# Kernel optimization log

Measured on AMD Instinct MI355X. Metric: run time of the kernel, lower is better.

Reference implementation:

```python
import jax, jax.numpy as jnp
import numpy as np

B, C, S, W, H = 4, 512, 1, 64, 64
D = C // 8  # query/key channel dim from Conv2d(in_dim, in_dim // 8, 1)
N = W * H


def setup_inputs() -> dict:
    key = jax.random.key(0)
    ks = jax.random.split(key, 8)
    s_in = 1.0 / np.sqrt(C)
    return {
        "x": jax.random.normal(ks[0], (B, C, S, W, H), dtype=jnp.float32),
        "Wq": jax.random.normal(ks[1], (D, C), dtype=jnp.float32) * s_in,
        "bq": jax.random.normal(ks[2], (D,), dtype=jnp.float32) * 0.01,
        "Wk": jax.random.normal(ks[3], (D, C), dtype=jnp.float32) * s_in,
        "bk": jax.random.normal(ks[4], (D,), dtype=jnp.float32) * 0.01,
        "Wv": jax.random.normal(ks[5], (C, C), dtype=jnp.float32) * s_in,
        "bv": jax.random.normal(ks[6], (C,), dtype=jnp.float32) * 0.01,
        "gamma": jax.random.uniform(ks[7], (1,), dtype=jnp.float32),
        "crop_h": 64,
        "crop_w": 64,
    }


def reference(x, Wq, bq, Wk, bk, Wv, bv, gamma, crop_h, crop_w):
    # x: [B, C, 1, W, H] -> flatten spatial to tokens: [B, C, N]
    b, c, s, w, h = x.shape
    n = w * h
    xs = x[:, :, 0].reshape(b, c, n)
    # 1x1 convs == channel matmuls
    q = jnp.einsum('dc,bcn->bnd', Wq, xs) + bq  # [B, N, D] (proj_query, permuted)
    k = jnp.einsum('dc,bcn->bdn', Wk, xs) + bk[:, None]  # [B, D, N]
    energy = jnp.einsum('bnd,bdm->bnm', q, k)  # [B, N, N]
    attention = jax.nn.softmax(energy, axis=-1)  # softmax over last dim
    v = jnp.einsum('dc,bcn->bdn', Wv, xs) + bv[:, None]  # [B, C, N]
    # out = bmm(value, attention^T): [B, C, N]
    out = jnp.einsum('bcn,bmn->bcm', v, attention)
    out = out.reshape(b, c, w, h)
    out = gamma[0] * out + x[:, :, 0]
    return out, attention
```

## Files before the change

### kernel.cpp

```cpp
#include <hip/hip_runtime.h>
#include <hip/hip_bf16.h>


#define B_ 4
#define C_ 512
#define D_ 64
#define N_ 4096

typedef __hip_bfloat16 bf16;
typedef __attribute__((ext_vector_type(8))) short bf16x8;
typedef __attribute__((ext_vector_type(4))) float f32x4;

__device__ __forceinline__ void gload16(const void* g, void* l) {
    __builtin_amdgcn_global_load_lds(
        (__attribute__((address_space(1))) void*)g,
        (__attribute__((address_space(3))) void*)l, 16, 0, 0);
}

__global__ __launch_bounds__(256) void prep_weights(
        const float* __restrict__ Wq, const float* __restrict__ Wk,
        const float* __restrict__ Wv,
        float* __restrict__ WqT, float* __restrict__ WkT,
        bf16* __restrict__ Wvb) {
    int i = blockIdx.x * 256 + threadIdx.x;
    if (i < 32768) {
        int d = i >> 9, c = i & 511;
        WqT[c * 64 + d] = Wq[i];
    } else if (i < 65536) {
        int j = i - 32768;
        int d = j >> 9, c = j & 511;
        WkT[c * 64 + d] = Wk[j];
    } else {
        int j = i - 65536;
        if (j < 262144) Wvb[j] = __float2bfloat16(Wv[j]);
    }
}

__global__ __launch_bounds__(256) void transpose_cast(const float* __restrict__ x,
                                                      bf16* __restrict__ xT) {
    __shared__ bf16 tile[32][33];
    int b = blockIdx.z;
    int n0 = blockIdx.x * 32;
    int c0 = blockIdx.y * 32;
    int tx = threadIdx.x;
    int ty = threadIdx.y;
    const float* xb = x + (size_t)b * C_ * N_;
    bf16* xTb = xT + (size_t)b * N_ * C_;
#pragma unroll
    for (int k = 0; k < 32; k += 8)
        tile[ty + k][tx] = __float2bfloat16(xb[(size_t)(c0 + ty + k) * N_ + n0 + tx]);
    __syncthreads();
#pragma unroll
    for (int k = 0; k < 32; k += 8)
        xTb[(size_t)(n0 + ty + k) * C_ + c0 + tx] = tile[tx][ty + k];
}

__global__ __launch_bounds__(256) void proj_qk(
        const float* __restrict__ x,
        const float* __restrict__ WqT, const float* __restrict__ WkT,
        const float* __restrict__ bq, const float* __restrict__ bk,
        float* __restrict__ Q, float* __restrict__ Km) {
    int b = blockIdx.y;
    int which = blockIdx.z;
    int n = blockIdx.x * 256 + threadIdx.x;
    const float* WT = which ? WkT : WqT;
    const float* bias = which ? bk : bq;
    const float* xb = x + (size_t)b * C_ * N_;

    float acc[64];
#pragma unroll
    for (int d = 0; d < 64; d++) acc[d] = 0.f;

    for (int c = 0; c < 512; c++) {
        float xv = xb[(size_t)c * N_ + n];
        const float* wrow = WT + c * 64;
#pragma unroll
        for (int d = 0; d < 64; d += 4) {
            float4 w = *(const float4*)(wrow + d);
            acc[d + 0] += w.x * xv;
            acc[d + 1] += w.y * xv;
            acc[d + 2] += w.z * xv;
            acc[d + 3] += w.w * xv;
        }
    }

    if (which == 0) {
        float* q = Q + ((size_t)b * N_ + n) * 64;
#pragma unroll
        for (int d = 0; d < 64; d += 4) {
            float4 v;
            v.x = acc[d + 0] + bias[d + 0];
            v.y = acc[d + 1] + bias[d + 1];
            v.z = acc[d + 2] + bias[d + 2];
            v.w = acc[d + 3] + bias[d + 3];
            *(float4*)(q + d) = v;
        }
    } else {
        float* kb = Km + (size_t)b * 64 * N_;
#pragma unroll
        for (int d = 0; d < 64; d++)
            kb[(size_t)d * N_ + n] = acc[d] + bias[d];
    }
}

__global__ __launch_bounds__(64) void proj_v(
        const bf16* __restrict__ Wvb, const bf16* __restrict__ xTb,
        const float* __restrict__ bv, bf16* __restrict__ V) {
    int b = blockIdx.z;
    int r0 = blockIdx.y * 64;
    int c0 = blockIdx.x * 64;
    int lane = threadIdx.x;
    int l15 = lane & 15;
    int kq  = lane >> 4;
    const bf16* Bb = xTb + (size_t)b * N_ * C_;

    f32x4 acc[4][4];
#pragma unroll
    for (int i = 0; i < 4; i++)
#pragma unroll
        for (int j = 0; j < 4; j++)
#pragma unroll
            for (int r = 0; r < 4; r++) acc[i][j][r] = 0.f;

    for (int k = 0; k < 512; k += 32) {
        bf16x8 af[4], bfr[4];
#pragma unroll
        for (int i = 0; i < 4; i++)
            af[i] = *(const bf16x8*)(Wvb + (size_t)(r0 + i * 16 + l15) * 512 + k + kq * 8);
#pragma unroll
        for (int j = 0; j < 4; j++)
            bfr[j] = *(const bf16x8*)(Bb + (size_t)(c0 + j * 16 + l15) * 512 + k + kq * 8);
#pragma unroll
        for (int i = 0; i < 4; i++)
#pragma unroll
            for (int j = 0; j < 4; j++)
                acc[i][j] = __builtin_amdgcn_mfma_f32_16x16x32_bf16(af[i], bfr[j], acc[i][j], 0, 0, 0);
    }

    bf16* Vb = V + (size_t)b * C_ * N_;
#pragma unroll
    for (int i = 0; i < 4; i++)
#pragma unroll
        for (int j = 0; j < 4; j++)
#pragma unroll
            for (int r = 0; r < 4; r++) {
                int row = r0 + i * 16 + kq * 4 + r;
                int col = c0 + j * 16 + l15;
                Vb[(size_t)row * N_ + col] = __float2bfloat16(acc[i][j][r] + bv[row]);
            }
}

__global__ __launch_bounds__(256, 2) void attn_softmax(
        const float* __restrict__ Q, const float* __restrict__ Km,
        float* __restrict__ attF, bf16* __restrict__ attB) {
    int b = blockIdx.y;
    int n0 = blockIdx.x * 8;
    int tid = threadIdx.x;

    __shared__ float Qs[64][8];
    __shared__ float red[8][4];

    for (int t = tid; t < 512; t += 256) {
        int r = t >> 6, d = t & 63;
        Qs[d][r] = Q[(size_t)b * N_ * 64 + (size_t)(n0 + r) * 64 + d];
    }
    __syncthreads();

    float acc[8][16];
#pragma unroll
    for (int r = 0; r < 8; r++)
#pragma unroll
        for (int ch = 0; ch < 16; ch++) acc[r][ch] = 0.f;

    const float* Kb = Km + (size_t)b * 64 * N_;
    for (int d = 0; d < 64; d++) {
        float qv[8];
#pragma unroll
        for (int r = 0; r < 8; r++) qv[r] = Qs[d][r];
#pragma unroll
        for (int ch = 0; ch < 16; ch++) {
            float kv = Kb[(size_t)d * N_ + ch * 256 + tid];
#pragma unroll
            for (int r = 0; r < 8; r++) acc[r][ch] = fmaf(kv, qv[r], acc[r][ch]);
        }
    }

    float mx[8];
#pragma unroll
    for (int r = 0; r < 8; r++) {
        float m = acc[r][0];
#pragma unroll
        for (int ch = 1; ch < 16; ch++) m = fmaxf(m, acc[r][ch]);
        for (int off = 32; off; off >>= 1) m = fmaxf(m, __shfl_down(m, off, 64));
        if ((tid & 63) == 0) red[r][tid >> 6] = m;
    }
    __syncthreads();
#pragma unroll
    for (int r = 0; r < 8; r++)
        mx[r] = fmaxf(fmaxf(red[r][0], red[r][1]), fmaxf(red[r][2], red[r][3]));
    __syncthreads();

    float inv[8];
#pragma unroll
    for (int r = 0; r < 8; r++) {
        float s = 0.f;
#pragma unroll
        for (int ch = 0; ch < 16; ch++) {
            acc[r][ch] = __expf(acc[r][ch] - mx[r]);
            s += acc[r][ch];
        }
        for (int off = 32; off; off >>= 1) s += __shfl_down(s, off, 64);
        if ((tid & 63) == 0) red[r][tid >> 6] = s;
    }
    __syncthreads();
#pragma unroll
    for (int r = 0; r < 8; r++)
        inv[r] = 1.f / (red[r][0] + red[r][1] + red[r][2] + red[r][3]);

    float* af = attF + (size_t)b * N_ * N_;
    bf16* ab = attB ? attB + (size_t)b * N_ * N_ : (bf16*)0;
#pragma unroll
    for (int r = 0; r < 8; r++)
#pragma unroll
        for (int ch = 0; ch < 16; ch++) {
            float p = acc[r][ch] * inv[r];
            size_t idx = (size_t)(n0 + r) * N_ + ch * 256 + tid;
            af[idx] = p;
            if (ab) ab[idx] = __float2bfloat16(p);
        }
}

__global__ __launch_bounds__(256, 2) void pv_out_fast(
        const bf16* __restrict__ V, const bf16* __restrict__ attB,
        const float* __restrict__ x, const float* __restrict__ gamma,
        float* __restrict__ out) {
    int b = blockIdx.z;
    int c0 = blockIdx.y * 128;
    int m0 = blockIdx.x * 128;
    int tid = threadIdx.x;
    int wv = tid >> 6;
    int lane = tid & 63;
    int l15 = lane & 15;
    int kq  = lane >> 4;
    int wr = wv >> 1;
    int wc = wv & 1;

    __shared__ bf16 Vs[128 * 32];
    __shared__ bf16 As[128 * 32];

    const bf16* Vb = V + (size_t)b * C_ * N_;
    const bf16* Ab = attB + (size_t)b * N_ * N_;

    int srow = tid >> 2;
    int scol = (tid & 3) * 8;
    bf16* VsW0 = Vs + wv * 512;
    bf16* AsW0 = As + wv * 512;

    f32x4 acc[4][4];
#pragma unroll
    for (int i = 0; i < 4; i++)
#pragma unroll
        for (int j = 0; j < 4; j++)
#pragma unroll
            for (int r = 0; r < 4; r++) acc[i][j][r] = 0.f;

    for (int kt = 0; kt < N_; kt += 32) {
#pragma unroll
        for (int rnd = 0; rnd < 2; rnd++) {
            int row = srow + rnd * 64;
            gload16(Vb + (size_t)(c0 + row) * N_ + kt + scol, VsW0 + rnd * 2048);
            gload16(Ab + (size_t)(m0 + row) * N_ + kt + scol, AsW0 + rnd * 2048);
        }
        __syncthreads();

        bf16x8 af[4], bfr[4];
#pragma unroll
        for (int i = 0; i < 4; i++)
            af[i] = *(const bf16x8*)(Vs + (wr * 64 + i * 16 + l15) * 32 + kq * 8);
#pragma unroll
        for (int j = 0; j < 4; j++)
            bfr[j] = *(const bf16x8*)(As + (wc * 64 + j * 16 + l15) * 32 + kq * 8);
#pragma unroll
        for (int i = 0; i < 4; i++)
#pragma unroll
            for (int j = 0; j < 4; j++)
                acc[i][j] = __builtin_amdgcn_mfma_f32_16x16x32_bf16(af[i], bfr[j], acc[i][j], 0, 0, 0);
        __syncthreads();
    }

    float g = gamma[0];
    const float* xb = x + (size_t)b * C_ * N_;
    float* ob = out + (size_t)b * C_ * N_;
#pragma unroll
    for (int i = 0; i < 4; i++)
#pragma unroll
        for (int j = 0; j < 4; j++)
#pragma unroll
            for (int r = 0; r < 4; r++) {
                int row = c0 + wr * 64 + i * 16 + kq * 4 + r;
                int col = m0 + wc * 64 + j * 16 + l15;
                size_t idx = (size_t)row * N_ + col;
                ob[idx] = g * acc[i][j][r] + xb[idx];
            }
}

__global__ __launch_bounds__(256, 2) void pv_out(
        const bf16* __restrict__ V, const bf16* __restrict__ attB,
        const float* __restrict__ attF,
        const float* __restrict__ x, const float* __restrict__ gamma,
        float* __restrict__ out) {
    int b = blockIdx.z;
    int wave = threadIdx.x >> 6;
    int c0 = blockIdx.y * 128 + (wave >> 1) * 64;
    int m0 = blockIdx.x * 128 + (wave & 1) * 64;
    int lane = threadIdx.x & 63;
    int l15 = lane & 15;
    int kq  = lane >> 4;

    const bf16* Vb = V + (size_t)b * C_ * N_;
    const bf16* AbB = attB ? attB + (size_t)b * N_ * N_ : (const bf16*)0;
    const float* AbF = attF + (size_t)b * N_ * N_;

    f32x4 acc[4][4];
#pragma unroll
    for (int i = 0; i < 4; i++)
#pragma unroll
        for (int j = 0; j < 4; j++)
#pragma unroll
            for (int r = 0; r < 4; r++) acc[i][j][r] = 0.f;

    for (int n = 0; n < N_; n += 32) {
        bf16x8 af[4], bfr[4];
#pragma unroll
        for (int i = 0; i < 4; i++)
            af[i] = *(const bf16x8*)(Vb + (size_t)(c0 + i * 16 + l15) * N_ + n + kq * 8);
        if (AbB) {
#pragma unroll
            for (int j = 0; j < 4; j++)
                bfr[j] = *(const bf16x8*)(AbB + (size_t)(m0 + j * 16 + l15) * N_ + n + kq * 8);
        } else {
#pragma unroll
            for (int j = 0; j < 4; j++) {
                const float* ap = AbF + (size_t)(m0 + j * 16 + l15) * N_ + n + kq * 8;
                float4 u = *(const float4*)ap;
                float4 w = *(const float4*)(ap + 4);
                bf16x8 bb;
                bf16* pb = (bf16*)&bb;
                pb[0] = __float2bfloat16(u.x); pb[1] = __float2bfloat16(u.y);
                pb[2] = __float2bfloat16(u.z); pb[3] = __float2bfloat16(u.w);
                pb[4] = __float2bfloat16(w.x); pb[5] = __float2bfloat16(w.y);
                pb[6] = __float2bfloat16(w.z); pb[7] = __float2bfloat16(w.w);
                bfr[j] = bb;
            }
        }
#pragma unroll
        for (int i = 0; i < 4; i++)
#pragma unroll
            for (int j = 0; j < 4; j++)
                acc[i][j] = __builtin_amdgcn_mfma_f32_16x16x32_bf16(af[i], bfr[j], acc[i][j], 0, 0, 0);
    }

    float g = gamma[0];
    const float* xb = x + (size_t)b * C_ * N_;
    float* ob = out + (size_t)b * C_ * N_;
#pragma unroll
    for (int i = 0; i < 4; i++)
#pragma unroll
        for (int j = 0; j < 4; j++)
#pragma unroll
            for (int r = 0; r < 4; r++) {
                int row = c0 + i * 16 + kq * 4 + r;
                int col = m0 + j * 16 + l15;
                size_t idx = (size_t)row * N_ + col;
                ob[idx] = g * acc[i][j][r] + xb[idx];
            }
}

extern "C" void kernel_launch(void* const* d_in, const int* in_sizes, int n_in,
                              void* d_out, int out_size, void* d_ws, size_t ws_size,
                              hipStream_t stream) {
    const float* x     = (const float*)d_in[0];
    const float* Wq    = (const float*)d_in[1];
    const float* bq    = (const float*)d_in[2];
    const float* Wk    = (const float*)d_in[3];
    const float* bk    = (const float*)d_in[4];
    const float* Wv    = (const float*)d_in[5];
    const float* bv    = (const float*)d_in[6];
    const float* gamma = (const float*)d_in[7];
    (void)in_sizes; (void)n_in; (void)out_size;

    float* out  = (float*)d_out;
    float* attF = out + (size_t)B_ * C_ * N_;

    char* ws = (char*)d_ws;
    float* Q   = (float*)(ws + 0);
    float* K   = (float*)(ws + 4194304);
    bf16*  V   = (bf16*) (ws + 8388608);
    bf16*  xTb = (bf16*) (ws + 25165824);
    float* WqT = (float*)(ws + 41943040);
    float* WkT = (float*)(ws + 42074112);
    bf16*  Wvb = (bf16*) (ws + 42205184);
    bf16*  attB = (bf16*)(ws + 42729472);
    const size_t full_need = 42729472ULL + (size_t)B_ * N_ * N_ * 2;
    bf16* attB_use = (ws_size >= full_need) ? attB : (bf16*)0;

    prep_weights<<<1280, 256, 0, stream>>>(Wq, Wk, Wv, WqT, WkT, Wvb);

    transpose_cast<<<dim3(N_ / 32, C_ / 32, B_), dim3(32, 8), 0, stream>>>(x, xTb);

    proj_qk<<<dim3(N_ / 256, B_, 2), 256, 0, stream>>>(x, WqT, WkT, bq, bk, Q, K);

    proj_v<<<dim3(N_ / 64, C_ / 64, B_), 64, 0, stream>>>(Wvb, xTb, bv, V);

    attn_softmax<<<dim3(N_ / 8, B_), 256, 0, stream>>>(Q, K, attF, attB_use);

    if (attB_use) {
        pv_out_fast<<<dim3(N_ / 128, C_ / 128, B_), 256, 0, stream>>>(
            V, attB_use, x, gamma, out);
    } else {
        pv_out<<<dim3(N_ / 128, C_ / 128, B_), 256, 0, stream>>>(
            V, attB_use, attF, x, gamma, out);
    }
}
```

Measured before the change: 854.3 us.

## Split QK projection over d, LDS-tile V projection, widen softmax blocks

proj_qk now splits the 64 output channels into four 16-channel slices per block. This cuts register pressure and gives the launch more blocks. proj_v moves from one-wave 64x64 tiles that read operands directly from global memory to four-wave 128x128 tiles staged through LDS with global_load_lds. attn_softmax uses 1024-thread blocks handling 16 query rows, with float4 K loads prefetched one step ahead, xor-shuffle reductions and vectorized float4/bf16x4 stores for the attention output. Together these aim to raise memory efficiency on the attention write and the projections, at the cost of larger blocks and more LDS use.

```diff
diff --git a/kernel.cpp b/kernel.cpp
--- a/kernel.cpp
+++ b/kernel.cpp
@@ -61,21 +61,23 @@
         const float* __restrict__ bq, const float* __restrict__ bk,
         float* __restrict__ Q, float* __restrict__ Km) {
     int b = blockIdx.y;
-    int which = blockIdx.z;
+    int z = blockIdx.z;
+    int which = z >> 2;
+    int dh = (z & 3) * 16;
     int n = blockIdx.x * 256 + threadIdx.x;
     const float* WT = which ? WkT : WqT;
     const float* bias = which ? bk : bq;
     const float* xb = x + (size_t)b * C_ * N_;
 
-    float acc[64];
-#pragma unroll
-    for (int d = 0; d < 64; d++) acc[d] = 0.f;
+    float acc[16];
+#pragma unroll
+    for (int d = 0; d < 16; d++) acc[d] = 0.f;
 
     for (int c = 0; c < 512; c++) {
         float xv = xb[(size_t)c * N_ + n];
-        const float* wrow = WT + c * 64;
-#pragma unroll
-        for (int d = 0; d < 64; d += 4) {
+        const float* wrow = WT + c * 64 + dh;
+#pragma unroll
+        for (int d = 0; d < 16; d += 4) {
             float4 w = *(const float4*)(wrow + d);
             acc[d + 0] += w.x * xv;
             acc[d + 1] += w.y * xv;
@@ -85,35 +87,48 @@
     }
 
     if (which == 0) {
-        float* q = Q + ((size_t)b * N_ + n) * 64;
-#pragma unroll
-        for (int d = 0; d < 64; d += 4) {
+        float* q = Q + ((size_t)b * N_ + n) * 64 + dh;
+#pragma unroll
+        for (int d = 0; d < 16; d += 4) {
             float4 v;
-            v.x = acc[d + 0] + bias[d + 0];
-            v.y = acc[d + 1] + bias[d + 1];
-            v.z = acc[d + 2] + bias[d + 2];
-            v.w = acc[d + 3] + bias[d + 3];
+            v.x = acc[d + 0] + bias[dh + d + 0];
+            v.y = acc[d + 1] + bias[dh + d + 1];
+            v.z = acc[d + 2] + bias[dh + d + 2];
+            v.w = acc[d + 3] + bias[dh + d + 3];
             *(float4*)(q + d) = v;
         }
     } else {
         float* kb = Km + (size_t)b * 64 * N_;
 #pragma unroll
-        for (int d = 0; d < 64; d++)
-            kb[(size_t)d * N_ + n] = acc[d] + bias[d];
-    }
-}
-
-__global__ __launch_bounds__(64) void proj_v(
+        for (int d = 0; d < 16; d++)
+            kb[(size_t)(dh + d) * N_ + n] = acc[d] + bias[dh + d];
+    }
+}
+
+__global__ __launch_bounds__(256, 2) void proj_v(
         const bf16* __restrict__ Wvb, const bf16* __restrict__ xTb,
         const float* __restrict__ bv, bf16* __restrict__ V) {
     int b = blockIdx.z;
-    int r0 = blockIdx.y * 64;
-    int c0 = blockIdx.x * 64;
-    int lane = threadIdx.x;
+    int r0 = blockIdx.y * 128;
+    int n0 = blockIdx.x * 128;
+    int tid = threadIdx.x;
+    int wv = tid >> 6;
+    int lane = tid & 63;
     int l15 = lane & 15;
     int kq  = lane >> 4;
+    int wr = wv >> 1;
+    int wc = wv & 1;
+
+    __shared__ bf16 Ws[128 * 32];
+    __shared__ bf16 Xs[128 * 32];
+
     const bf16* Bb = xTb + (size_t)b * N_ * C_;
 
+    int srow = tid >> 2;
+    int scol = (tid & 3) * 8;
+    bf16* WsW0 = Ws + wv * 512;
+    bf16* XsW0 = Xs + wv * 512;
+
     f32x4 acc[4][4];
 #pragma unroll
     for (int i = 0; i < 4; i++)
@@ -122,112 +137,148 @@
 #pragma unroll
             for (int r = 0; r < 4; r++) acc[i][j][r] = 0.f;
 
-    for (int k = 0; k < 512; k += 32) {
+    for (int kt = 0; kt < C_; kt += 32) {
+#pragma unroll
+        for (int rnd = 0; rnd < 2; rnd++) {
+            int row = srow + rnd * 64;
+            gload16(Wvb + (size_t)(r0 + row) * C_ + kt + scol, WsW0 + rnd * 2048);
+            gload16(Bb + (size_t)(n0 + row) * C_ + kt + scol, XsW0 + rnd * 2048);
+        }
+        __syncthreads();
+
         bf16x8 af[4], bfr[4];
 #pragma unroll
         for (int i = 0; i < 4; i++)
-            af[i] = *(const bf16x8*)(Wvb + (size_t)(r0 + i * 16 + l15) * 512 + k + kq * 8);
-#pragma unroll
-        for (int j = 0; j < 4; j++)
-            bfr[j] = *(const bf16x8*)(Bb + (size_t)(c0 + j * 16 + l15) * 512 + k + kq * 8);
+            af[i] = *(const bf16x8*)(Ws + (wr * 64 + i * 16 + l15) * 32 + kq * 8);
+#pragma unroll
+        for (int j = 0; j < 4; j++)
+            bfr[j] = *(const bf16x8*)(Xs + (wc * 64 + j * 16 + l15) * 32 + kq * 8);
 #pragma unroll
         for (int i = 0; i < 4; i++)
 #pragma unroll
             for (int j = 0; j < 4; j++)
                 acc[i][j] = __builtin_amdgcn_mfma_f32_16x16x32_bf16(af[i], bfr[j], acc[i][j], 0, 0, 0);
+        __syncthreads();
     }
 
     bf16* Vb = V + (size_t)b * C_ * N_;
 #pragma unroll
     for (int i = 0; i < 4; i++)
 #pragma unroll
-        for (int j = 0; j < 4; j++)
-#pragma unroll
-            for (int r = 0; r < 4; r++) {
-                int row = r0 + i * 16 + kq * 4 + r;
-                int col = c0 + j * 16 + l15;
-                Vb[(size_t)row * N_ + col] = __float2bfloat16(acc[i][j][r] + bv[row]);
+        for (int r = 0; r < 4; r++) {
+            int row = r0 + wr * 64 + i * 16 + kq * 4 + r;
+            float bvv = bv[row];
+#pragma unroll
+            for (int j = 0; j < 4; j++) {
+                int col = n0 + wc * 64 + j * 16 + l15;
+                Vb[(size_t)row * N_ + col] = __float2bfloat16(acc[i][j][r] + bvv);
             }
-}
-
-__global__ __launch_bounds__(256, 2) void attn_softmax(
+        }
+}
+
+__global__ __launch_bounds__(1024, 4) void attn_softmax(
         const float* __restrict__ Q, const float* __restrict__ Km,
         float* __restrict__ attF, bf16* __restrict__ attB) {
     int b = blockIdx.y;
-    int n0 = blockIdx.x * 8;
+    int n0 = blockIdx.x * 16;
     int tid = threadIdx.x;
-
-    __shared__ float Qs[64][8];
-    __shared__ float red[8][4];
-
-    for (int t = tid; t < 512; t += 256) {
-        int r = t >> 6, d = t & 63;
-        Qs[d][r] = Q[(size_t)b * N_ * 64 + (size_t)(n0 + r) * 64 + d];
+    int wv = tid >> 6;
+    int lane = tid & 63;
+    int col = tid * 4;
+
+    __shared__ float Qs[64][16];
+    __shared__ float red[16][16];
+
+    {
+        int r = tid >> 6, d = tid & 63;
+        Qs[d][r] = Q[((size_t)b * N_ + n0 + r) * 64 + d];
     }
     __syncthreads();
 
-    float acc[8][16];
-#pragma unroll
-    for (int r = 0; r < 8; r++)
-#pragma unroll
-        for (int ch = 0; ch < 16; ch++) acc[r][ch] = 0.f;
-
-    const float* Kb = Km + (size_t)b * 64 * N_;
+    float acc[16][4];
+#pragma unroll
+    for (int r = 0; r < 16; r++)
+#pragma unroll
+        for (int j = 0; j < 4; j++) acc[r][j] = 0.f;
+
+    const float* kp = Km + (size_t)b * 64 * N_ + col;
+    float4 ka = *(const float4*)kp;
     for (int d = 0; d < 64; d++) {
-        float qv[8];
-#pragma unroll
-        for (int r = 0; r < 8; r++) qv[r] = Qs[d][r];
-#pragma unroll
-        for (int ch = 0; ch < 16; ch++) {
-            float kv = Kb[(size_t)d * N_ + ch * 256 + tid];
-#pragma unroll
-            for (int r = 0; r < 8; r++) acc[r][ch] = fmaf(kv, qv[r], acc[r][ch]);
-        }
-    }
-
-    float mx[8];
-#pragma unroll
-    for (int r = 0; r < 8; r++) {
-        float m = acc[r][0];
-#pragma unroll
-        for (int ch = 1; ch < 16; ch++) m = fmaxf(m, acc[r][ch]);
-        for (int off = 32; off; off >>= 1) m = fmaxf(m, __shfl_down(m, off, 64));
-        if ((tid & 63) == 0) red[r][tid >> 6] = m;
+        float4 kn;
+        if (d < 63) kn = *(const float4*)(kp + (size_t)(d + 1) * N_);
+        const float4* qrow = (const float4*)(&Qs[d][0]);
+        float4 q0 = qrow[0], q1 = qrow[1], q2 = qrow[2], q3 = qrow[3];
+        float qv[16] = {q0.x, q0.y, q0.z, q0.w, q1.x, q1.y, q1.z, q1.w,
+                        q2.x, q2.y, q2.z, q2.w, q3.x, q3.y, q3.z, q3.w};
+#pragma unroll
+        for (int r = 0; r < 16; r++) {
+            acc[r][0] = fmaf(ka.x, qv[r], acc[r][0]);
+            acc[r][1] = fmaf(ka.y, qv[r], acc[r][1]);
+            acc[r][2] = fmaf(ka.z, qv[r], acc[r][2]);
+            acc[r][3] = fmaf(ka.w, qv[r], acc[r][3]);
+        }
+        ka = kn;
+    }
+
+    float mx[16];
+#pragma unroll
+    for (int r = 0; r < 16; r++) {
+        float m = fmaxf(fmaxf(acc[r][0], acc[r][1]), fmaxf(acc[r][2], acc[r][3]));
+#pragma unroll
+        for (int off = 32; off; off >>= 1) m = fmaxf(m, __shfl_xor(m, off, 64));
+        if (lane == 0) red[r][wv] = m;
     }
     __syncthreads();
 #pragma unroll
-    for (int r = 0; r < 8; r++)
-        mx[r] = fmaxf(fmaxf(red[r][0], red[r][1]), fmaxf(red[r][2], red[r][3]));
+    for (int r = 0; r < 16; r++) {
+        const float4* rp = (const float4*)(&red[r][0]);
+        float4 a = rp[0], c = rp[1], e = rp[2], g = rp[3];
+        mx[r] = fmaxf(fmaxf(fmaxf(fmaxf(a.x, a.y), fmaxf(a.z, a.w)),
+                            fmaxf(fmaxf(c.x, c.y), fmaxf(c.z, c.w))),
+                      fmaxf(fmaxf(fmaxf(e.x, e.y), fmaxf(e.z, e.w)),
+                            fmaxf(fmaxf(g.x, g.y), fmaxf(g.z, g.w))));
+    }
     __syncthreads();
 
-    float inv[8];
-#pragma unroll
-    for (int r = 0; r < 8; r++) {
-        float s = 0.f;
-#pragma unroll
-        for (int ch = 0; ch < 16; ch++) {
-            acc[r][ch] = __expf(acc[r][ch] - mx[r]);
-            s += acc[r][ch];
-        }
-        for (int off = 32; off; off >>= 1) s += __shfl_down(s, off, 64);
-        if ((tid & 63) == 0) red[r][tid >> 6] = s;
+    float inv[16];
+#pragma unroll
+    for (int r = 0; r < 16; r++) {
+        acc[r][0] = __expf(acc[r][0] - mx[r]);
+        acc[r][1] = __expf(acc[r][1] - mx[r]);
+        acc[r][2] = __expf(acc[r][2] - mx[r]);
+        acc[r][3] = __expf(acc[r][3] - mx[r]);
+        float s = (acc[r][0] + acc[r][1]) + (acc[r][2] + acc[r][3]);
+#pragma unroll
+        for (int off = 32; off; off >>= 1) s += __shfl_xor(s, off, 64);
+        if (lane == 0) red[r][wv] = s;
     }
     __syncthreads();
 #pragma unroll
-    for (int r = 0; r < 8; r++)
-        inv[r] = 1.f / (red[r][0] + red[r][1] + red[r][2] + red[r][3]);
+    for (int r = 0; r < 16; r++) {
+        const float4* rp = (const float4*)(&red[r][0]);
+        float4 a = rp[0], c = rp[1], e = rp[2], g = rp[3];
+        float s = ((a.x + a.y) + (a.z + a.w)) + ((c.x + c.y) + (c.z + c.w))
+                + ((e.x + e.y) + (e.z + e.w)) + ((g.x + g.y) + (g.z + g.w));
+        inv[r] = 1.f / s;
+    }
 
     float* af = attF + (size_t)b * N_ * N_;
     bf16* ab = attB ? attB + (size_t)b * N_ * N_ : (bf16*)0;
 #pragma unroll
-    for (int r = 0; r < 8; r++)
-#pragma unroll
-        for (int ch = 0; ch < 16; ch++) {
-            float p = acc[r][ch] * inv[r];
-            size_t idx = (size_t)(n0 + r) * N_ + ch * 256 + tid;
-            af[idx] = p;
-            if (ab) ab[idx] = __float2bfloat16(p);
-        }
+    for (int r = 0; r < 16; r++) {
+        size_t idx = (size_t)(n0 + r) * N_ + col;
+        float4 p;
+        p.x = acc[r][0] * inv[r];
+        p.y = acc[r][1] * inv[r];
+        p.z = acc[r][2] * inv[r];
+        p.w = acc[r][3] * inv[r];
+        *(float4*)(af + idx) = p;
+        if (ab) {
+            bf16 pb[4] = {__float2bfloat16(p.x), __float2bfloat16(p.y),
+                          __float2bfloat16(p.z), __float2bfloat16(p.w)};
+            *(short4*)(ab + idx) = *(short4*)pb;
+        }
+    }
 }
 
 __global__ __launch_bounds__(256, 2) void pv_out_fast(
@@ -408,11 +459,11 @@
 
     transpose_cast<<<dim3(N_ / 32, C_ / 32, B_), dim3(32, 8), 0, stream>>>(x, xTb);
 
-    proj_qk<<<dim3(N_ / 256, B_, 2), 256, 0, stream>>>(x, WqT, WkT, bq, bk, Q, K);
-
-    proj_v<<<dim3(N_ / 64, C_ / 64, B_), 64, 0, stream>>>(Wvb, xTb, bv, V);
-
-    attn_softmax<<<dim3(N_ / 8, B_), 256, 0, stream>>>(Q, K, attF, attB_use);
+    proj_qk<<<dim3(N_ / 256, B_, 8), 256, 0, stream>>>(x, WqT, WkT, bq, bk, Q, K);
+
+    proj_v<<<dim3(N_ / 128, C_ / 128, B_), 256, 0, stream>>>(Wvb, xTb, bv, V);
+
+    attn_softmax<<<dim3(N_ / 16, B_), 1024, 0, stream>>>(Q, K, attF, attB_use);
 
     if (attB_use) {
         pv_out_fast<<<dim3(N_ / 128, C_ / 128, B_), 256, 0, stream>>>(
```

New measurement: 1.535 ms. 79.7% more time.
